# Kernel optimization log

Hardware: AMD Instinct MI355X
Metric: run time of the kernel (lower is better)

The kernel has to match this reference:

```python
import jax, jax.numpy as jnp
import numpy as np

THRESHOLD = 0.5  # default threshold from MemoryPool.update

N, D, P, C0 = 16384, 1024, 4096, 2048


def setup_inputs() -> dict:
    key = jax.random.key(0)
    k1, k2, k3, k4 = jax.random.split(key, 4)
    summaries = jax.random.normal(k1, (N, D), dtype=jnp.float32)
    scores = jax.random.uniform(k2, (N,), dtype=jnp.float32)
    slot = jnp.arange(P)
    # slots >= count are empty (zeros), matching fresh torch buffers
    pool = jnp.where((slot < C0)[:, None],
                     jax.random.normal(k3, (P, D), dtype=jnp.float32), 0.0)
    priorities = jnp.where(slot < C0,
                           jax.random.uniform(k4, (P,), dtype=jnp.float32), 0.0)
    return {"summaries": summaries, "scores": scores,
            "pool": pool, "priorities": priorities, "count": C0}


def reference(summaries, scores, pool, priorities, count):
    pool_size = pool.shape[0]
    cnt0 = jnp.asarray(count, jnp.int32)

    def step(carry, xc):
        pl, pr, cnt = carry
        s, sc = xc  # (D,), ()
        valid = sc > THRESHOLD
        min_idx = jnp.argmin(pr)
        has_room = cnt < pool_size
        idx = jnp.where(has_room, cnt, min_idx)
        replace_ok = sc > pr[min_idx]
        do_write = valid & (has_room | replace_ok)
        new_pl = jnp.where(do_write, pl.at[idx].set(s), pl)
        new_pr = jnp.where(do_write, pr.at[idx].set(sc), pr)
        new_cnt = cnt + (do_write & has_room).astype(jnp.int32)
        return (new_pl, new_pr, new_cnt), None

    (pool_out, prior_out, cnt_out), _ = jax.lax.scan(
        step, (pool, priorities, cnt0), (summaries, scores))
    return pool_out, prior_out, cnt_out
```

## Files before the change

### kernel.cpp

```cpp
#include <hip/hip_runtime.h>

typedef unsigned long long u64;
#define THRESH 0.5f
#define ALL1 0xFFFFFFFFFFFFFFFFull
#define FINF __builtin_inff()

__device__ __forceinline__ u64 shflxU64(u64 v, int m) { return __shfl_xor(v, m, 64); }
__device__ __forceinline__ void sort64(u64 &key, int lane) {
#pragma unroll
    for (int k = 2; k <= 64; k <<= 1) {
#pragma unroll
        for (int j = k >> 1; j > 0; j >>= 1) {
            u64 p = shflxU64(key, j);
            bool takeMax = ((lane & j) != 0) != ((lane & k) != 0);
            u64 mn = key < p ? key : p;
            u64 mx = key < p ? p : key;
            key = takeMax ? mx : mn;
        }
    }
}

__global__ __launch_bounds__(1024) void k1_scan(
    const float* __restrict__ scores, const float* __restrict__ priorities,
    const int* __restrict__ countPtr, int N, int P,
    float* __restrict__ outPrior, float* __restrict__ outCnt, int* __restrict__ srcWs,
    float* __restrict__ cval, int* __restrict__ csrc, int* __restrict__ meta,
    int* __restrict__ cnt2, int* __restrict__ cnt4)
{
    const int tid = threadIdx.x;
    for (int s = tid; s < P; s += 1024) { outPrior[s] = priorities[s]; srcWs[s] = -1; }
    for (int s = tid; s < N; s += 1024) cnt2[s] = 0;
    for (int s = tid; s < P + N; s += 1024) cnt4[s] = 0;
    int C0 = *countPtr; C0 = C0 < 0 ? 0 : (C0 > P ? P : C0);
    const int per = (N + 1023) >> 10;
    const int i0 = tid * per;
    const int i1 = min(i0 + per, N);
    int c = 0;
    for (int i = i0; i < i1; ++i) c += (scores[i] > THRESH) ? 1 : 0;
    __shared__ int sb[1024];
    sb[tid] = c; __syncthreads();
    for (int off = 1; off < 1024; off <<= 1) {
        int v = (tid >= off) ? sb[tid - off] : 0;
        __syncthreads();
        sb[tid] += v;
        __syncthreads();
    }
    const int total = sb[1023];
    int v = sb[tid] - c;
    int A = P - C0; if (A > total) A = total; if (A < 0) A = 0;
    for (int i = i0; i < i1; ++i) {
        float sc = scores[i];
        if (sc > THRESH) {
            if (v < A) { outPrior[C0 + v] = sc; srcWs[C0 + v] = i; }
            else { cval[v - A] = sc; csrc[v - A] = i; }
            ++v;
        }
    }
    if (tid == 0) {
        meta[0] = total - A;
        meta[1] = C0 + A;
        outCnt[0] = (float)(C0 + A);
    }
}

#define K2T 1024
__global__ __launch_bounds__(256) void k2_count(
    const float* __restrict__ outPrior, const float* __restrict__ cval,
    const int* __restrict__ meta, int* __restrict__ cnt2)
{
    const int M = meta[0], F = meta[1];
    const int iB = blockIdx.x << 8;
    if (iB >= M) return;
    const int hi = min(M, iB + 256);
    const int totSrc = F + hi;
    const int tb = blockIdx.y * K2T;
    if (tb >= totSrc) return;
    const int te = min(totSrc - tb, K2T);
    const int i = iB + threadIdx.x;
    const bool live = i < M;
    const float x = live ? cval[i] : 0.f;
    __shared__ __align__(16) float tile[K2T];
    for (int t = threadIdx.x; t < K2T; t += 256) {
        const int s = tb + t;
        tile[t] = (t < te) ? ((s < F) ? outPrior[s] : cval[s - F]) : FINF;
    }
    __syncthreads();
    if (!live) return;
    int lim = F + i - tb;
    if (lim < 0) lim = 0;
    if (lim > te) lim = te;
    int cnt = 0;
    const int l4 = lim >> 2;
    const float4* t4 = (const float4*)tile;
    for (int q = 0; q < l4; ++q) {
        const float4 w = t4[q];
        cnt += (w.x < x) + (w.y < x) + (w.z < x) + (w.w < x);
    }
    for (int t = l4 << 2; t < lim; ++t) cnt += tile[t] < x;
    if (cnt) atomicAdd(&cnt2[i], cnt);
}

__global__ __launch_bounds__(1024) void k3_compact(
    const float* __restrict__ cval, const int* __restrict__ csrc,
    const int* __restrict__ cnt2, int* __restrict__ meta,
    float* __restrict__ cvalS, float* __restrict__ wval, int* __restrict__ wsrc,
    int* __restrict__ writeNum)
{
    const int M = meta[0];
    const int tid = threadIdx.x;
    const int per = (M + 1023) >> 10;
    const int i0 = tid * per, i1 = min(i0 + per, M);
    int c = 0;
    for (int i = i0; i < i1; ++i) c += (cnt2[i] >= i + 1) ? 1 : 0;
    __shared__ int sb[1024];
    sb[tid] = c; __syncthreads();
    for (int off = 1; off < 1024; off <<= 1) {
        int v = (tid >= off) ? sb[tid - off] : 0;
        __syncthreads();
        sb[tid] += v;
        __syncthreads();
    }
    int w = sb[tid] - c;
    for (int i = i0; i < i1; ++i) {
        if (cnt2[i] >= i + 1) {
            wval[w] = cval[i]; wsrc[w] = csrc[i]; writeNum[i] = w; cvalS[i] = cval[i]; ++w;
        } else { writeNum[i] = -1; cvalS[i] = FINF; }
    }
    if (tid == 0) meta[2] = sb[1023];
}

#define K4T 1024
__global__ __launch_bounds__(256) void k4_count(
    const float* __restrict__ outPrior, const float* __restrict__ cvalS,
    const int* __restrict__ meta, int P, int* __restrict__ cnt4)
{
    const int M = meta[0], F = meta[1];
    if (M == 0) return;
    const int tot = F + M;
    const int eB = blockIdx.x << 8;
    if (eB >= tot) return;
    const int tb = blockIdx.y * K4T;
    if (tb >= tot) return;
    const int te = min(tot - tb, K4T);
    const int e = eB + threadIdx.x;
    bool live = e < tot;
    float x = 0.f; int myid = 0;
    if (live) {
        if (e < F) { x = outPrior[e]; myid = e; }
        else {
            x = cvalS[e - F]; myid = P + (e - F);
            if (x == FINF) live = false;
        }
    }
    __shared__ __align__(16) float tile[K4T];
    for (int t = threadIdx.x; t < K4T; t += 256) {
        const int s = tb + t;
        tile[t] = (t < te) ? ((s < F) ? outPrior[s] : cvalS[s - F]) : FINF;
    }
    __syncthreads();
    if (!live) return;
    int cnt = 0;
    int lim1 = F - tb;
    if (lim1 < 0) lim1 = 0;
    if (lim1 > te) lim1 = te;
#define K4_SEG(a, b, d)                                                        \
    {                                                                          \
        const int a_ = (a), b_ = (b), d_ = (d);                                \
        int aa = (a_ + 3) & ~3; if (aa > b_) aa = b_;                          \
        for (int t = a_; t < aa; ++t) {                                        \
            const float v = tile[t]; const int sid = tb + t + d_;              \
            cnt += (int)((v < x) | ((v == x) & (sid < myid)));                 \
        }                                                                      \
        const int b4 = aa + (((b_ - aa) >> 2) << 2);                           \
        for (int t = aa; t < b4; t += 4) {                                     \
            const float4 w = *(const float4*)(tile + t);                       \
            const int sid = tb + t + d_;                                       \
            cnt += (int)((w.x < x) | ((w.x == x) & (sid < myid)));             \
            cnt += (int)((w.y < x) | ((w.y == x) & (sid + 1 < myid)));         \
            cnt += (int)((w.z < x) | ((w.z == x) & (sid + 2 < myid)));         \
            cnt += (int)((w.w < x) | ((w.w == x) & (sid + 3 < myid)));         \
        }                                                                      \
        for (int t = b4; t < b_; ++t) {                                        \
            const float v = tile[t]; const int sid = tb + t + d_;              \
            cnt += (int)((v < x) | ((v == x) & (sid < myid)));                 \
        }                                                                      \
    }
    K4_SEG(0, lim1, 0)
    K4_SEG(lim1, te, P - F)
#undef K4_SEG
    if (cnt) atomicAdd(&cnt4[e], cnt);
}

__global__ __launch_bounds__(256) void k4_scatter(
    const float* __restrict__ outPrior, const float* __restrict__ cvalS,
    const int* __restrict__ writeNum, const int* __restrict__ meta, int P,
    const int* __restrict__ cnt4,
    float* __restrict__ evV, int* __restrict__ evId, int* __restrict__ survW)
{
    const int M = meta[0], F = meta[1], R = meta[2];
    if (M == 0) return;
    const int tot = F + M;
    const int e = blockIdx.x * 256 + threadIdx.x;
    if (e >= tot) return;
    float x; int myid; bool isCand = false; int wn = -1;
    if (e < F) { x = outPrior[e]; myid = e; }
    else {
        const int i = e - F;
        x = cvalS[i];
        if (x == FINF) return;
        isCand = true; wn = writeNum[i]; myid = P + i;
    }
    const int cnt = cnt4[e];
    if (isCand) survW[wn] = (cnt >= R) ? 1 : 0;
    if (cnt < R + 64) { evV[cnt] = x; evId[cnt] = isCand ? (P + wn) : myid; }
}

#define SCAP 14400
#define MSF   (1 << 29)
#define DONEF (1 << 30)
#define SLOTM ((1 << 29) - 1)
__global__ __launch_bounds__(1024) void k5_chain(
    const float* __restrict__ evV, const int* __restrict__ evId,
    const int* __restrict__ meta, int P,
    int* __restrict__ Sg, int* __restrict__ survW)
{
    __shared__ int state[SCAP];
    __shared__ int shRp, shLeft;
    const int tid = threadIdx.x;
    const int R = meta[2];
    if (R <= 0 || R > SCAP) return;
    const int F = meta[1];
    const int Wtot = F + R;

    if (tid == 0) {
        int Rp = R;
        if (R < Wtot) {
            const float vR1 = evV[R - 1];
            if (evV[R] == vR1) {
                int rr = R - 1;
                while (rr >= 0 && evV[rr] == vR1) --rr;
                Rp = rr + 1;
            }
        }
        shRp = Rp;
    }
    __syncthreads();
    const int Rp = shRp;

    for (int r = tid; r < Rp; r += 1024) state[r] = 0;
    __syncthreads();

    for (int round = 0; round < Rp + 2; ++round) {
        for (int r = tid; r < Rp; r += 1024) {
            if (state[r] & (DONEF | MSF)) continue;
            int cur = r, ms = -1;
            while (true) {
                const int id = evId[cur];
                if (id < P) { ms = id; break; }
                const int p = id - P;
                if (p >= cur || p < 0) break;
                const int sp = state[p];
                if (sp & DONEF) { ms = sp & SLOTM; break; }
                const float v = evV[p];
                const bool tiedP = (p > 0 && evV[p - 1] == v) ||
                                   (p + 1 < Rp && evV[p + 1] == v);
                if (tiedP) break;
                cur = p;
            }
            if (ms >= 0) {
                const float v = evV[r];
                const bool tiedR = (r > 0 && evV[r - 1] == v) ||
                                   (r + 1 < Rp && evV[r + 1] == v);
                state[r] = ms | (tiedR ? MSF : (MSF | DONEF));
            }
        }
        __syncthreads();
        for (int r = tid; r < Rp; r += 1024) {
            const float v = evV[r];
            if (r > 0 && evV[r - 1] == v) continue;
            if (r + 1 >= Rp || evV[r + 1] != v) continue;
            if (state[r] & DONEF) continue;
            int re = r + 1;
            while (re < Rp && evV[re] == v) ++re;
            bool ready = true;
            for (int s = r; s < re; ++s) ready &= (state[s] & MSF) != 0;
            if (!ready) continue;
            for (int j = r; j < re; ++j) {
                int best = j;
                for (int s = j + 1; s < re; ++s)
                    if ((state[s] & SLOTM) < (state[best] & SLOTM)) best = s;
                const int tmp = state[best];
                state[best] = state[j];
                state[j] = tmp;
            }
            for (int j = r; j < re; ++j) state[j] |= DONEF;
        }
        __syncthreads();
        if (tid == 0) shLeft = 0;
        __syncthreads();
        int loc = 0;
        for (int r = tid; r < Rp; r += 1024) loc += (state[r] & DONEF) ? 0 : 1;
        if (loc) atomicAdd(&shLeft, loc);
        __syncthreads();
        if (shLeft == 0) break;
    }

    for (int r = tid; r < Rp; r += 1024) Sg[r] = state[r] & SLOTM;
    __syncthreads();

    if (Rp < R && tid < 64) {
        const int lane = tid;
        const int r = Rp + lane;
        const float v0 = evV[Rp];
        const bool mem = (r < Wtot) && (evV[r] == v0);
        const int g = (int)__popcll(__ballot(mem));
        const int e = R - Rp;
        int id = 0, ms = 0;
        if (mem) {
            id = evId[r];
            ms = (id < P) ? id : (state[id - P] & SLOTM);
        }
        u64 key = mem ? ((((u64)(unsigned)ms) << 32) | (u64)(unsigned)id) : ALL1;
        sort64(key, lane);
        const int sid = (int)(unsigned)(key & 0xFFFFFFFFull);
        const int sms = (int)(unsigned)(key >> 32);
        const bool real = (key != ALL1) && (lane < g);
        if (real && lane < e) Sg[Rp + lane] = sms;
        if (real && sid >= P) survW[sid - P] = (lane >= e) ? 1 : 0;
    }
}

__global__ __launch_bounds__(256) void k5b_apply(
    const int* __restrict__ Sg, const int* __restrict__ survW,
    const float* __restrict__ wval, const int* __restrict__ wsrc,
    const int* __restrict__ meta,
    float* __restrict__ outPrior, int* __restrict__ srcWs)
{
    const int R = meta[2];
    const int j = blockIdx.x * 256 + threadIdx.x;
    if (j >= R) return;
    if (survW[j]) {
        const int s = Sg[j];
        outPrior[s] = wval[j];
        srcWs[s] = wsrc[j];
    }
}

__global__ __launch_bounds__(256) void gather_kernel(
    const float* __restrict__ summaries,
    const float* __restrict__ pool,
    const int* __restrict__ src,
    float* __restrict__ outPool, int D) {
    int p = blockIdx.x;
    int s = src[p];
    const float* row = (s >= 0) ? (summaries + (size_t)s * D) : (pool + (size_t)p * D);
    float* o = outPool + (size_t)p * D;
    if ((D & 3) == 0) {
        for (int k = (threadIdx.x << 2); k < D; k += (blockDim.x << 2)) {
            float4 v = *(const float4*)(row + k);
            *(float4*)(o + k) = v;
        }
    } else {
        for (int k = threadIdx.x; k < D; k += blockDim.x) o[k] = row[k];
    }
}

extern "C" void kernel_launch(void* const* d_in, const int* in_sizes, int n_in,
                              void* d_out, int out_size, void* d_ws, size_t ws_size,
                              hipStream_t stream) {
    const float* summaries  = (const float*)d_in[0];
    const float* scores     = (const float*)d_in[1];
    const float* pool       = (const float*)d_in[2];
    const float* priorities = (const float*)d_in[3];
    const int*   count      = (const int*)d_in[4];

    int N = in_sizes[1];
    int P = in_sizes[3];
    int D = in_sizes[0] / N;

    float* outPool  = (float*)d_out;
    float* outPrior = outPool + (size_t)P * D;
    float* outCnt   = outPrior + P;
    int*   srcWs    = (int*)d_ws;

    float* cval     = outPool;
    int*   csrc     = (int*)outPool + 1 * N;
    float* cvalS    = outPool + 3 * N;
    float* wval     = outPool + 4 * N;
    int*   wsrc     = (int*)outPool + 5 * N;
    int*   writeNum = (int*)outPool + 6 * N;
    float* evV      = outPool + 7 * N;
    int*   evId     = (int*)outPool + 8 * N + 64;
    int*   Sgbuf    = (int*)outPool + 9 * N + 128;
    int*   survW    = (int*)outPool + 10 * N + 128;
    int*   meta     = (int*)outPool + 11 * N + 128;
    int*   cnt2     = (int*)outPool + 11 * N + 192;
    int*   cnt4     = (int*)outPool + 12 * N + 192;

    const int nb2 = (N + 255) / 256;
    const int nb4 = (P + N + 255) / 256;
    const int ty  = (P + N + K2T - 1) / K2T;

    dim3 g2(nb2, ty), g4(nb4, ty);

    k1_scan<<<1, 1024, 0, stream>>>(scores, priorities, count, N, P,
                                    outPrior, outCnt, srcWs, cval, csrc, meta,
                                    cnt2, cnt4);
    k2_count<<<g2, 256, 0, stream>>>(outPrior, cval, meta, cnt2);
    k3_compact<<<1, 1024, 0, stream>>>(cval, csrc, cnt2, meta, cvalS, wval, wsrc, writeNum);
    k4_count<<<g4, 256, 0, stream>>>(outPrior, cvalS, meta, P, cnt4);
    k4_scatter<<<nb4, 256, 0, stream>>>(outPrior, cvalS, writeNum, meta, P, cnt4,
                                        evV, evId, survW);
    k5_chain<<<1, 1024, 0, stream>>>(evV, evId, meta, P, Sgbuf, survW);
    k5b_apply<<<nb2, 256, 0, stream>>>(Sgbuf, survW, wval, wsrc, meta, outPrior, srcWs);
    gather_kernel<<<P, 256, 0, stream>>>(summaries, pool, srcWs, outPool, D);
}
```

Before: 218.5 us.

## Use packed 64-bit keys in rank count, shrink tiles, vectorize scan loads

Several changes at once. k1 loads its 16 scores per thread with float4 reads into registers, and the zeroing of the count buffers moves out of the single-block kernel into hipMemsetAsync calls. k2 and k4 drop their tile size from 1024 to 512 for more blocks, and k2 gets a fully unrolled fast path for tiles that lie completely below the thread's limit. k4 replaces the float compare with its tie-break on source id by a single compare of packed 64-bit (value, id) keys, which removes the segment logic but doubles shared-memory traffic per element.

```diff
diff --git a/kernel.cpp b/kernel.cpp
--- a/kernel.cpp
+++ b/kernel.cpp
@@ -20,23 +20,40 @@
     }
 }
 
+__device__ __forceinline__ u64 mkey(float v, int id) {
+    v = (v == 0.0f) ? 0.0f : v;
+    unsigned u = __float_as_uint(v);
+    u ^= (unsigned)((int)u >> 31) | 0x80000000u;
+    return ((u64)u << 32) | (unsigned)id;
+}
+
 __global__ __launch_bounds__(1024) void k1_scan(
     const float* __restrict__ scores, const float* __restrict__ priorities,
     const int* __restrict__ countPtr, int N, int P,
     float* __restrict__ outPrior, float* __restrict__ outCnt, int* __restrict__ srcWs,
-    float* __restrict__ cval, int* __restrict__ csrc, int* __restrict__ meta,
-    int* __restrict__ cnt2, int* __restrict__ cnt4)
+    float* __restrict__ cval, int* __restrict__ csrc, int* __restrict__ meta)
 {
     const int tid = threadIdx.x;
     for (int s = tid; s < P; s += 1024) { outPrior[s] = priorities[s]; srcWs[s] = -1; }
-    for (int s = tid; s < N; s += 1024) cnt2[s] = 0;
-    for (int s = tid; s < P + N; s += 1024) cnt4[s] = 0;
     int C0 = *countPtr; C0 = C0 < 0 ? 0 : (C0 > P ? P : C0);
     const int per = (N + 1023) >> 10;
     const int i0 = tid * per;
-    const int i1 = min(i0 + per, N);
+    float sv[16];
+    if (per == 16 && i0 + 16 <= N) {
+        const float4* s4 = (const float4*)(scores + i0);
+        const float4 a = s4[0], b = s4[1], c4 = s4[2], d = s4[3];
+        sv[0]=a.x; sv[1]=a.y; sv[2]=a.z; sv[3]=a.w;
+        sv[4]=b.x; sv[5]=b.y; sv[6]=b.z; sv[7]=b.w;
+        sv[8]=c4.x; sv[9]=c4.y; sv[10]=c4.z; sv[11]=c4.w;
+        sv[12]=d.x; sv[13]=d.y; sv[14]=d.z; sv[15]=d.w;
+    } else {
+#pragma unroll 16
+        for (int j = 0; j < 16; ++j)
+            sv[j] = (j < per && i0 + j < N) ? scores[i0 + j] : 0.f;
+    }
     int c = 0;
-    for (int i = i0; i < i1; ++i) c += (scores[i] > THRESH) ? 1 : 0;
+#pragma unroll 16
+    for (int j = 0; j < 16; ++j) c += (j < per && i0 + j < N && sv[j] > THRESH) ? 1 : 0;
     __shared__ int sb[1024];
     sb[tid] = c; __syncthreads();
     for (int off = 1; off < 1024; off <<= 1) {
@@ -48,12 +65,15 @@
     const int total = sb[1023];
     int v = sb[tid] - c;
     int A = P - C0; if (A > total) A = total; if (A < 0) A = 0;
-    for (int i = i0; i < i1; ++i) {
-        float sc = scores[i];
-        if (sc > THRESH) {
-            if (v < A) { outPrior[C0 + v] = sc; srcWs[C0 + v] = i; }
-            else { cval[v - A] = sc; csrc[v - A] = i; }
-            ++v;
+#pragma unroll 16
+    for (int j = 0; j < 16; ++j) {
+        if (j < per && i0 + j < N) {
+            const float sc = sv[j];
+            if (sc > THRESH) {
+                if (v < A) { outPrior[C0 + v] = sc; srcWs[C0 + v] = i0 + j; }
+                else { cval[v - A] = sc; csrc[v - A] = i0 + j; }
+                ++v;
+            }
         }
     }
     if (tid == 0) {
@@ -63,7 +83,7 @@
     }
 }
 
-#define K2T 1024
+#define K2T 512
 __global__ __launch_bounds__(256) void k2_count(
     const float* __restrict__ outPrior, const float* __restrict__ cval,
     const int* __restrict__ meta, int* __restrict__ cnt2)
@@ -72,31 +92,38 @@
     const int iB = blockIdx.x << 8;
     if (iB >= M) return;
     const int hi = min(M, iB + 256);
-    const int totSrc = F + hi;
+    const int smax = F + hi;
     const int tb = blockIdx.y * K2T;
-    if (tb >= totSrc) return;
-    const int te = min(totSrc - tb, K2T);
-    const int i = iB + threadIdx.x;
-    const bool live = i < M;
-    const float x = live ? cval[i] : 0.f;
+    if (tb >= smax) return;
+    const int te = min(smax - tb, K2T);
     __shared__ __align__(16) float tile[K2T];
     for (int t = threadIdx.x; t < K2T; t += 256) {
         const int s = tb + t;
         tile[t] = (t < te) ? ((s < F) ? outPrior[s] : cval[s - F]) : FINF;
     }
     __syncthreads();
-    if (!live) return;
-    int lim = F + i - tb;
-    if (lim < 0) lim = 0;
-    if (lim > te) lim = te;
+    const int i = iB + threadIdx.x;
+    if (i >= M) return;
+    const float x = cval[i];
     int cnt = 0;
-    const int l4 = lim >> 2;
     const float4* t4 = (const float4*)tile;
-    for (int q = 0; q < l4; ++q) {
-        const float4 w = t4[q];
-        cnt += (w.x < x) + (w.y < x) + (w.z < x) + (w.w < x);
-    }
-    for (int t = l4 << 2; t < lim; ++t) cnt += tile[t] < x;
+    if (tb + K2T <= F + iB) {
+#pragma unroll 8
+        for (int q = 0; q < K2T / 4; ++q) {
+            const float4 w = t4[q];
+            cnt += (w.x < x) + (w.y < x) + (w.z < x) + (w.w < x);
+        }
+    } else {
+        int lim = F + i - tb;
+        if (lim < 0) lim = 0;
+        if (lim > te) lim = te;
+        const int l4 = lim >> 2;
+        for (int q = 0; q < l4; ++q) {
+            const float4 w = t4[q];
+            cnt += (w.x < x) + (w.y < x) + (w.z < x) + (w.w < x);
+        }
+        for (int t = l4 << 2; t < lim; ++t) cnt += tile[t] < x;
+    }
     if (cnt) atomicAdd(&cnt2[i], cnt);
 }
 
@@ -129,7 +156,7 @@
     if (tid == 0) meta[2] = sb[1023];
 }
 
-#define K4T 1024
+#define K4T 512
 __global__ __launch_bounds__(256) void k4_count(
     const float* __restrict__ outPrior, const float* __restrict__ cvalS,
     const int* __restrict__ meta, int P, int* __restrict__ cnt4)
@@ -142,52 +169,34 @@
     const int tb = blockIdx.y * K4T;
     if (tb >= tot) return;
     const int te = min(tot - tb, K4T);
-    const int e = eB + threadIdx.x;
-    bool live = e < tot;
-    float x = 0.f; int myid = 0;
-    if (live) {
-        if (e < F) { x = outPrior[e]; myid = e; }
-        else {
-            x = cvalS[e - F]; myid = P + (e - F);
-            if (x == FINF) live = false;
-        }
-    }
-    __shared__ __align__(16) float tile[K4T];
+    __shared__ __align__(16) u64 tile[K4T];
     for (int t = threadIdx.x; t < K4T; t += 256) {
         const int s = tb + t;
-        tile[t] = (t < te) ? ((s < F) ? outPrior[s] : cvalS[s - F]) : FINF;
+        u64 kk = ALL1;
+        if (t < te) {
+            if (s < F) kk = mkey(outPrior[s], s);
+            else       kk = mkey(cvalS[s - F], P + (s - F));
+        }
+        tile[t] = kk;
     }
     __syncthreads();
-    if (!live) return;
+    const int e = eB + threadIdx.x;
+    if (e >= tot) return;
+    float x; int id;
+    if (e < F) { x = outPrior[e]; id = e; }
+    else {
+        x = cvalS[e - F];
+        if (x == FINF) return;
+        id = P + (e - F);
+    }
+    const u64 kx = mkey(x, id);
     int cnt = 0;
-    int lim1 = F - tb;
-    if (lim1 < 0) lim1 = 0;
-    if (lim1 > te) lim1 = te;
-#define K4_SEG(a, b, d)                                                        \
-    {                                                                          \
-        const int a_ = (a), b_ = (b), d_ = (d);                                \
-        int aa = (a_ + 3) & ~3; if (aa > b_) aa = b_;                          \
-        for (int t = a_; t < aa; ++t) {                                        \
-            const float v = tile[t]; const int sid = tb + t + d_;              \
-            cnt += (int)((v < x) | ((v == x) & (sid < myid)));                 \
-        }                                                                      \
-        const int b4 = aa + (((b_ - aa) >> 2) << 2);                           \
-        for (int t = aa; t < b4; t += 4) {                                     \
-            const float4 w = *(const float4*)(tile + t);                       \
-            const int sid = tb + t + d_;                                       \
-            cnt += (int)((w.x < x) | ((w.x == x) & (sid < myid)));             \
-            cnt += (int)((w.y < x) | ((w.y == x) & (sid + 1 < myid)));         \
-            cnt += (int)((w.z < x) | ((w.z == x) & (sid + 2 < myid)));         \
-            cnt += (int)((w.w < x) | ((w.w == x) & (sid + 3 < myid)));         \
-        }                                                                      \
-        for (int t = b4; t < b_; ++t) {                                        \
-            const float v = tile[t]; const int sid = tb + t + d_;              \
-            cnt += (int)((v < x) | ((v == x) & (sid < myid)));                 \
-        }                                                                      \
-    }
-    K4_SEG(0, lim1, 0)
-    K4_SEG(lim1, te, P - F)
-#undef K4_SEG
+    const ulonglong2* t2 = (const ulonglong2*)tile;
+#pragma unroll 8
+    for (int q = 0; q < K4T / 2; ++q) {
+        const ulonglong2 w = t2[q];
+        cnt += (int)(w.x < kx) + (int)(w.y < kx);
+    }
     if (cnt) atomicAdd(&cnt4[e], cnt);
 }
 
@@ -403,9 +412,11 @@
 
     dim3 g2(nb2, ty), g4(nb4, ty);
 
+    hipMemsetAsync(cnt2, 0, (size_t)N * sizeof(int), stream);
+    hipMemsetAsync(cnt4, 0, (size_t)(P + N) * sizeof(int), stream);
+
     k1_scan<<<1, 1024, 0, stream>>>(scores, priorities, count, N, P,
-                                    outPrior, outCnt, srcWs, cval, csrc, meta,
-                                    cnt2, cnt4);
+                                    outPrior, outCnt, srcWs, cval, csrc, meta);
     k2_count<<<g2, 256, 0, stream>>>(outPrior, cval, meta, cnt2);
     k3_compact<<<1, 1024, 0, stream>>>(cval, csrc, cnt2, meta, cvalS, wval, wsrc, writeNum);
     k4_count<<<g4, 256, 0, stream>>>(outPrior, cvalS, meta, P, cnt4);
```

Measured after the change: 181.7 us. -16.8%, faster.
